# Kernel optimization log

Measured on AMD Instinct MI355X. Metric: run time of the kernel, lower is better.

The kernel has to match this reference:

```python
import jax, jax.numpy as jnp
import numpy as np

DIM = 512
DIM_HEAD = 64
HEADS = 8
SCALE = 8.0  # Attend(scale=8)
DIM_INNER = DIM_HEAD * HEADS


def setup_inputs() -> dict:
    key = jax.random.key(0)
    k1, k2, k3, k4 = jax.random.split(key, 4)
    b, n = 8, 4096
    x = jax.random.normal(k1, (b, n, DIM), dtype=jnp.float32)
    gamma = jnp.ones((DIM,), dtype=jnp.float32)
    w_qkv = jax.random.normal(k2, (DIM, 3 * DIM_INNER), dtype=jnp.float32) * (DIM ** -0.5)
    temperature = jnp.ones((HEADS, 1, 1), dtype=jnp.float32)
    w_out = jax.random.normal(k3, (DIM_INNER, DIM), dtype=jnp.float32) * (DIM_INNER ** -0.5)
    return {"x": x, "gamma": gamma, "w_qkv": w_qkv, "temperature": temperature, "w_out": w_out}


def _l2norm(t, axis=-1, eps=1e-12):
    return t / jnp.maximum(jnp.linalg.norm(t, axis=axis, keepdims=True), eps)


def reference(x, gamma, w_qkv, temperature, w_out):
    b, n, _ = x.shape
    # RMSNorm: F.normalize(x, dim=-1) * sqrt(dim) * gamma
    xn = _l2norm(x) * (DIM ** 0.5) * gamma
    qkv = xn @ w_qkv                                   # [b, n, 3*h*d]
    qkv = qkv.reshape(b, n, 3, HEADS, DIM_HEAD)
    qkv = jnp.transpose(qkv, (2, 0, 3, 4, 1))          # [3, b, h, d, n]
    q, k, v = qkv[0], qkv[1], qkv[2]
    q = _l2norm(q)                                     # l2norm over n (last dim)
    k = _l2norm(k)
    q = q * jnp.exp(temperature)                       # [h,1,1] broadcast
    sim = jnp.einsum('bhdn,bhen->bhde', q, k) * SCALE  # [b, h, d, d]
    attn = jax.nn.softmax(sim, axis=-1)
    out = jnp.einsum('bhde,bhen->bhdn', attn, v)       # [b, h, d, n]
    out = jnp.transpose(out, (0, 3, 1, 2)).reshape(b, n, DIM_INNER)
    return out @ w_out
```

## Files before the change

kernel.cpp:

```cpp
#include <hip/hip_runtime.h>
#include <stdint.h>

#define NDIM 512
#define HEADS 8
#define DHEAD 64
#define NSEQ 4096
#define BATCH 8
#define ROWS (BATCH * NSEQ)
#define QKVN (3 * NDIM)

typedef unsigned short ushort_t;
typedef __bf16 bf16x8 __attribute__((ext_vector_type(8)));
typedef float f32x4 __attribute__((ext_vector_type(4)));
typedef unsigned short u16x8 __attribute__((ext_vector_type(8)));
typedef unsigned short u16x4 __attribute__((ext_vector_type(4)));

__device__ __forceinline__ ushort_t f2bf(float f) {
  union { float f; uint32_t u; } v; v.f = f;
  uint32_t r = (v.u + 0x7FFFu + ((v.u >> 16) & 1u)) >> 16;
  return (ushort_t)r;
}
__device__ __forceinline__ float bf2f(ushort_t h) {
  union { uint32_t u; float f; } v; v.u = ((uint32_t)h) << 16;
  return v.f;
}

__device__ __forceinline__ void gload_lds16(const void* g, void* l) {
  __builtin_amdgcn_global_load_lds(
      (__attribute__((address_space(1))) void*)(g),
      (__attribute__((address_space(3))) void*)(l), 16, 0, 0);
}

__global__ __launch_bounds__(256) void prep_k(const float* __restrict__ w_qkv,
                                              const float* __restrict__ w_out,
                                              ushort_t* __restrict__ wqkvT,
                                              ushort_t* __restrict__ woutT) {
  __shared__ float tile[32][33];
  int id = blockIdx.x;
  const float* src;
  ushort_t* dst;
  int srcStride, ni, ki;
  if (id < 768) {
    ni = id % 48; ki = id / 48; src = w_qkv; dst = wqkvT; srcStride = QKVN;
  } else {
    id -= 768;
    ni = id % 16; ki = id / 16; src = w_out; dst = woutT; srcStride = NDIM;
  }
  int tr = threadIdx.x >> 3;
  int tc = (threadIdx.x & 7) * 4;
  float4 v = *(const float4*)(src + (size_t)(ki * 32 + tr) * srcStride + ni * 32 + tc);
  tile[tr][tc] = v.x; tile[tr][tc + 1] = v.y; tile[tr][tc + 2] = v.z; tile[tr][tc + 3] = v.w;
  __syncthreads();
  u16x4 o;
  o[0] = f2bf(tile[tc + 0][tr]);
  o[1] = f2bf(tile[tc + 1][tr]);
  o[2] = f2bf(tile[tc + 2][tr]);
  o[3] = f2bf(tile[tc + 3][tr]);
  *(u16x4*)(dst + (size_t)(ni * 32 + tr) * NDIM + ki * 32 + tc) = o;
}

__global__ __launch_bounds__(256) void rmsnorm_k(const float* __restrict__ x,
                                                 const float* __restrict__ gamma,
                                                 ushort_t* __restrict__ xn) {
  int wave = threadIdx.x >> 6, lane = threadIdx.x & 63;
  size_t row = (size_t)blockIdx.x * 4 + wave;
  const float4* xr = (const float4*)(x + row * NDIM);
  float4 v0 = xr[lane * 2], v1 = xr[lane * 2 + 1];
  float s = v0.x*v0.x + v0.y*v0.y + v0.z*v0.z + v0.w*v0.w
          + v1.x*v1.x + v1.y*v1.y + v1.z*v1.z + v1.w*v1.w;
#pragma unroll
  for (int off = 32; off; off >>= 1) s += __shfl_xor(s, off, 64);
  float scale = 22.627416997969522f / fmaxf(sqrtf(s), 1e-12f);
  const float4* gr = (const float4*)gamma;
  float4 g0 = gr[lane * 2], g1 = gr[lane * 2 + 1];
  u16x8 o;
  o[0] = f2bf(v0.x * scale * g0.x);
  o[1] = f2bf(v0.y * scale * g0.y);
  o[2] = f2bf(v0.z * scale * g0.z);
  o[3] = f2bf(v0.w * scale * g0.w);
  o[4] = f2bf(v1.x * scale * g1.x);
  o[5] = f2bf(v1.y * scale * g1.y);
  o[6] = f2bf(v1.z * scale * g1.z);
  o[7] = f2bf(v1.w * scale * g1.w);
  *(u16x8*)(xn + row * NDIM + lane * 8) = o;
}

template <bool OUT_BF16>
__device__ __forceinline__ void gemm256x128_core(
    const ushort_t* __restrict__ A, size_t strideA, size_t m0,
    const ushort_t* __restrict__ B,
    void* __restrict__ C, size_t strideC, size_t n0,
    ushort_t* sm) {
  const int tid  = threadIdx.x;
  const int lane = tid & 63;
  const int wave = tid >> 6;
  const int srow = lane >> 3;
  const int scol = ((lane & 7) ^ srow) * 16;
  const int r = lane & 15, q = lane >> 4;
  const int wm = (wave >> 1) * 64;
  const int wn = (wave & 1) * 64;

  ushort_t* As = sm;
  ushort_t* Bs = sm + 49152;

  auto stageA = [&](int t2, int g) {
    gload_lds16((const char*)(A + (m0 + (size_t)(g * 8 + srow)) * strideA + t2 * 64) + scol,
                (char*)(As + (t2 % 3) * 16384 + g * 512));
  };
  auto stageB = [&](int t2, int g) {
    gload_lds16((const char*)(B + (size_t)(g * 8 + srow) * NDIM + t2 * 64) + scol,
                (char*)(Bs + (t2 % 3) * 8192 + g * 512));
  };

#pragma unroll
  for (int t2 = 0; t2 < 2; ++t2) {
#pragma unroll
    for (int a = 0; a < 4; ++a) stageA(t2, wave * 4 + a);
#pragma unroll
    for (int bb = 0; bb < 2; ++bb) stageB(t2, wave * 2 + bb);
  }
  asm volatile("s_waitcnt vmcnt(6)" ::: "memory");
  __builtin_amdgcn_s_barrier();

  f32x4 acc[4][4] = {};

#pragma unroll
  for (int t = 0; t < 8; ++t) {
    const ushort_t* Ab = As + (t % 3) * 16384;
    const ushort_t* Bb = Bs + (t % 3) * 8192;
#pragma unroll
    for (int ph = 0; ph < 2; ++ph) {
      const int kb = ph * 4 + q;
      bf16x8 af[4], bfr[4];
#pragma unroll
      for (int i = 0; i < 4; ++i) {
        int row = wm + i * 16 + r;
        af[i] = *(const bf16x8*)(const void*)(Ab + row * 64 + ((kb ^ (row & 7)) << 3));
      }
#pragma unroll
      for (int j = 0; j < 4; ++j) {
        int row = wn + j * 16 + r;
        bfr[j] = *(const bf16x8*)(const void*)(Bb + row * 64 + ((kb ^ (row & 7)) << 3));
      }
      if (t < 6) {
        int t2 = t + 2;
        if (ph == 0) { stageA(t2, wave * 4 + 0); stageA(t2, wave * 4 + 1); stageB(t2, wave * 2 + 0); }
        else         { stageA(t2, wave * 4 + 2); stageA(t2, wave * 4 + 3); stageB(t2, wave * 2 + 1); }
      }
      __builtin_amdgcn_s_barrier();
      asm volatile("s_waitcnt lgkmcnt(0)" ::: "memory");
      __builtin_amdgcn_s_setprio(1);
#pragma unroll
      for (int i = 0; i < 4; ++i)
#pragma unroll
        for (int j = 0; j < 4; ++j)
          acc[i][j] = __builtin_amdgcn_mfma_f32_16x16x32_bf16(af[i], bfr[j], acc[i][j], 0, 0, 0);
      __builtin_amdgcn_s_setprio(0);
      if (ph == 1) {
        if (t < 6)       { asm volatile("s_waitcnt vmcnt(6)" ::: "memory"); }
        else if (t == 6) { asm volatile("s_waitcnt vmcnt(0)" ::: "memory"); }
      }
      __builtin_amdgcn_s_barrier();
    }
  }

  __syncthreads();
  if constexpr (OUT_BF16) {
    ushort_t* Cb = sm;
    ushort_t* Cc = (ushort_t*)C;
#pragma unroll
    for (int i = 0; i < 4; ++i)
#pragma unroll
      for (int j = 0; j < 4; ++j)
#pragma unroll
        for (int v = 0; v < 4; ++v)
          Cb[(wm + i * 16 + q * 4 + v) * 136 + wn + j * 16 + r] = f2bf(acc[i][j][v]);
    __syncthreads();
#pragma unroll
    for (int it = 0; it < 8; ++it) {
      int row = (tid >> 4) + it * 32;
      int col = (tid & 15) * 8;
      u16x8 val = *(const u16x8*)(Cb + row * 136 + col);
      *(u16x8*)(Cc + (m0 + row) * strideC + n0 + col) = val;
    }
  } else {
    float* Cf = (float*)sm;
    float* Co = (float*)C;
#pragma unroll
    for (int p = 0; p < 2; ++p) {
      __syncthreads();
      if (((wave >> 2) & 1) == p) {
#pragma unroll
        for (int i = 0; i < 4; ++i)
#pragma unroll
          for (int j = 0; j < 4; ++j)
#pragma unroll
            for (int v = 0; v < 4; ++v)
              Cf[((wm & 127) + i * 16 + q * 4 + v) * 132 + wn + j * 16 + r] = acc[i][j][v];
      }
      __syncthreads();
      int row = tid >> 2;
      int c0 = (tid & 3) * 4;
#pragma unroll
      for (int it = 0; it < 8; ++it) {
        int col = c0 + it * 16;
        f32x4 val = *(const f32x4*)(Cf + row * 132 + col);
        *(f32x4*)(Co + (m0 + p * 128 + row) * strideC + n0 + col) = val;
      }
    }
  }
}

__global__ __launch_bounds__(512, 2) void gemm_qkv(const ushort_t* __restrict__ A,
                                                   const ushort_t* __restrict__ BT,
                                                   ushort_t* __restrict__ C) {
  __shared__ __align__(16) ushort_t sm[73728];
  const int flat = blockIdx.x;
  const int xcd = flat & 7;
  const int idx = flat >> 3;
  const int local_m = idx / 12;
  const int n_t = idx - local_m * 12;
  const size_t m0 = (size_t)(xcd * 16 + local_m) * 256;
  const size_t n0 = (size_t)n_t * 128;
  gemm256x128_core<true>(A, NDIM, m0, BT + n0 * NDIM, C, QKVN, n0, sm);
}

__global__ __launch_bounds__(256) void gram_k(const ushort_t* __restrict__ qkv,
                                              float* __restrict__ pG,
                                              float* __restrict__ pSq) {
  int chunk = blockIdx.x;
  int bh = blockIdx.y;
  int b = bh >> 3, h = bh & 7;
  __shared__ ushort_t Qt[64 * 72];
  __shared__ ushort_t Kt[64 * 72];
  __shared__ float sq[128];
  int tid = threadIdx.x, lane = tid & 63, wave = tid >> 6;
  int nl = tid >> 2;
  int dp = (tid & 3) * 16;
  int r = lane & 15, q = lane >> 4;
  float aq[16] = {}, ak[16] = {};
  f32x4 acc[4] = {};
  size_t base_row = ((size_t)b * NSEQ + (size_t)chunk * 512) * QKVN + (size_t)h * DHEAD;
  int swz_n = ((nl >> 3) & 7);
  int c_lo = (nl & 7) | (((swz_n ^ (dp >> 3)) & 7) << 3);
  int c_hi = (nl & 7) | (((swz_n ^ ((dp >> 3) + 1)) & 7) << 3);
  ushort_t* qlo = Qt + dp * 72 + c_lo;
  ushort_t* qhi = Qt + (dp + 8) * 72 + c_hi;
  ushort_t* klo = Kt + dp * 72 + c_lo;
  ushort_t* khi = Kt + (dp + 8) * 72 + c_hi;

  for (int sc = 0; sc < 8; ++sc) {
    __syncthreads();
    size_t g = base_row + (size_t)(sc * 64 + nl) * QKVN;
    u16x8 qv0 = *(const u16x8*)(qkv + g + dp);
    u16x8 qv1 = *(const u16x8*)(qkv + g + dp + 8);
    u16x8 kv0 = *(const u16x8*)(qkv + g + NDIM + dp);
    u16x8 kv1 = *(const u16x8*)(qkv + g + NDIM + dp + 8);
#pragma unroll
    for (int i = 0; i < 8; ++i) {
      float fq = bf2f(qv0[i]); aq[i] += fq * fq;       qlo[i * 72] = qv0[i];
      float fq2 = bf2f(qv1[i]); aq[8 + i] += fq2 * fq2; qhi[i * 72] = qv1[i];
      float fk = bf2f(kv0[i]); ak[i] += fk * fk;       klo[i * 72] = kv0[i];
      float fk2 = bf2f(kv1[i]); ak[8 + i] += fk2 * fk2; khi[i * 72] = kv1[i];
    }
    __syncthreads();
#pragma unroll
    for (int ks = 0; ks < 64; ks += 32) {
      int kb = (ks >> 3) + q;
      int m = wave * 16 + r;
      bf16x8 a = *(const bf16x8*)(const void*)(Qt + m * 72 + (((kb ^ (m >> 3)) & 7) << 3));
#pragma unroll
      for (int j = 0; j < 4; ++j) {
        int e = j * 16 + r;
        bf16x8 bb = *(const bf16x8*)(const void*)(Kt + e * 72 + (((kb ^ (e >> 3)) & 7) << 3));
        acc[j] = __builtin_amdgcn_mfma_f32_16x16x32_bf16(a, bb, acc[j], 0, 0, 0);
      }
    }
  }
  size_t gbase = ((size_t)bh * 8 + chunk) * 4096;
#pragma unroll
  for (int j = 0; j < 4; ++j)
#pragma unroll
    for (int v = 0; v < 4; ++v)
      pG[gbase + (size_t)(wave * 16 + q * 4 + v) * 64 + j * 16 + r] = acc[j][v];
  if (tid < 128) sq[tid] = 0.f;
  __syncthreads();
#pragma unroll
  for (int i = 0; i < 16; ++i) {
    atomicAdd(&sq[dp + i], aq[i]);
    atomicAdd(&sq[64 + dp + i], ak[i]);
  }
  __syncthreads();
  if (tid < 128) pSq[((size_t)bh * 8 + chunk) * 128 + tid] = sq[tid];
}

__global__ __launch_bounds__(256) void softmax_k(const float* __restrict__ pG,
                                                 const float* __restrict__ pSq,
                                                 const float* __restrict__ temp,
                                                 ushort_t* __restrict__ attnT) {
  int bh = blockIdx.x;
  int h = bh & 7;
  int t = threadIdx.x;
  int d = t >> 2;
  int eg = (t & 3) * 16;
  __shared__ float kn[64];
  if (t < 64) {
    float sk = 0.f;
    for (int c = 0; c < 8; ++c) sk += pSq[((size_t)bh * 8 + c) * 128 + 64 + t];
    kn[t] = fmaxf(sqrtf(sk), 1e-12f);
  }
  float sq = 0.f;
  for (int c = 0; c < 8; ++c) sq += pSq[((size_t)bh * 8 + c) * 128 + d];
  float qn = fmaxf(sqrtf(sq), 1e-12f);
  __syncthreads();
  float scale = 8.0f * expf(temp[h]) / qn;
  float row[16];
#pragma unroll
  for (int k = 0; k < 16; ++k) row[k] = 0.f;
  for (int c = 0; c < 8; ++c) {
    const float4* src = (const float4*)(pG + ((size_t)bh * 8 + c) * 4096 + d * 64 + eg);
#pragma unroll
    for (int k4 = 0; k4 < 4; ++k4) {
      float4 v = src[k4];
      row[k4 * 4 + 0] += v.x; row[k4 * 4 + 1] += v.y;
      row[k4 * 4 + 2] += v.z; row[k4 * 4 + 3] += v.w;
    }
  }
#pragma unroll
  for (int k = 0; k < 16; ++k) row[k] = row[k] * scale / kn[eg + k];
  float mx = -1e30f;
#pragma unroll
  for (int k = 0; k < 16; ++k) mx = fmaxf(mx, row[k]);
  mx = fmaxf(mx, __shfl_xor(mx, 1, 64));
  mx = fmaxf(mx, __shfl_xor(mx, 2, 64));
  float s = 0.f;
#pragma unroll
  for (int k = 0; k < 16; ++k) { row[k] = expf(row[k] - mx); s += row[k]; }
  s += __shfl_xor(s, 1, 64);
  s += __shfl_xor(s, 2, 64);
  float inv = 1.0f / s;
#pragma unroll
  for (int k = 0; k < 16; ++k)
    attnT[(size_t)bh * 4096 + (eg + k) * 64 + d] = f2bf(row[k] * inv);
}

__global__ __launch_bounds__(256) void w2t_k(const ushort_t* __restrict__ woutT,
                                             const ushort_t* __restrict__ attnT,
                                             ushort_t* __restrict__ W2T) {
  int mq = blockIdx.x;
  int bh = blockIdx.y;
  int b = bh >> 3, h = bh & 7;
  int tid = threadIdx.x, lane = tid & 63, wave = tid >> 6;
  int r = lane & 15, q = lane >> 4;
  int mbase = mq * 128 + wave * 32;
  const ushort_t* At = attnT + (size_t)bh * 4096;
  f32x4 acc[2][4] = {};
#pragma unroll
  for (int kk = 0; kk < 64; kk += 32) {
    bf16x8 a[2], bb[4];
#pragma unroll
    for (int mf = 0; mf < 2; ++mf)
      a[mf] = *(const bf16x8*)(woutT + (size_t)(mbase + mf * 16 + r) * NDIM + h * 64 + kk + q * 8);
#pragma unroll
    for (int nf = 0; nf < 4; ++nf)
      bb[nf] = *(const bf16x8*)(At + (nf * 16 + r) * 64 + kk + q * 8);
#pragma unroll
    for (int mf = 0; mf < 2; ++mf)
#pragma unroll
      for (int nf = 0; nf < 4; ++nf)
        acc[mf][nf] = __builtin_amdgcn_mfma_f32_16x16x32_bf16(a[mf], bb[nf], acc[mf][nf], 0, 0, 0);
  }
#pragma unroll
  for (int mf = 0; mf < 2; ++mf)
#pragma unroll
    for (int nf = 0; nf < 4; ++nf)
#pragma unroll
      for (int v = 0; v < 4; ++v)
        W2T[(size_t)b * 262144 + (size_t)(mbase + mf * 16 + q * 4 + v) * NDIM +
            h * 64 + nf * 16 + r] = f2bf(acc[mf][nf][v]);
}

__global__ __launch_bounds__(512, 2) void gemm_v(const ushort_t* __restrict__ qkv,
                                                 const ushort_t* __restrict__ W2T,
                                                 float* __restrict__ out) {
  __shared__ __align__(16) ushort_t sm[73728];
  const int flat = blockIdx.x;
  const int b = flat & 7;
  const int local = flat >> 3;
  const int mt = local >> 2, nt = local & 3;
  const size_t m0 = (size_t)b * NSEQ + (size_t)mt * 256;
  const size_t n0 = (size_t)nt * 128;
  gemm256x128_core<false>(qkv + 1024, QKVN, m0,
                          W2T + (size_t)b * 262144 + n0 * NDIM,
                          out, NDIM, n0, sm);
}

extern "C" void kernel_launch(void* const* d_in, const int* in_sizes, int n_in,
                              void* d_out, int out_size, void* d_ws, size_t ws_size,
                              hipStream_t stream) {
  (void)in_sizes; (void)n_in; (void)out_size; (void)ws_size;
  const float* x     = (const float*)d_in[0];
  const float* gamma = (const float*)d_in[1];
  const float* w_qkv = (const float*)d_in[2];
  const float* temp  = (const float*)d_in[3];
  const float* w_out = (const float*)d_in[4];
  float* out = (float*)d_out;
  char* ws = (char*)d_ws;

  ushort_t* qkv   = (ushort_t*)ws;
  ushort_t* xn    = (ushort_t*)(ws + (size_t)100663296);
  float*    pG    = (float*)(ws + (size_t)100663296);
  float*    pSq   = (float*)(ws + (size_t)100663296 + 8388608);
  ushort_t* W2T   = (ushort_t*)(ws + (size_t)100663296 + 12582912);
  ushort_t* wqkvT = (ushort_t*)(ws + (size_t)134217728);
  ushort_t* woutT = (ushort_t*)(ws + (size_t)134217728 + 1572864);
  ushort_t* attnT = (ushort_t*)(ws + (size_t)134217728 + 2097152);

  prep_k<<<1024, 256, 0, stream>>>(w_qkv, w_out, wqkvT, woutT);
  rmsnorm_k<<<ROWS / 4, 256, 0, stream>>>(x, gamma, xn);
  gemm_qkv<<<(QKVN / 128) * (ROWS / 256), 512, 0, stream>>>(xn, wqkvT, qkv);
  gram_k<<<dim3(8, 64), 256, 0, stream>>>(qkv, pG, pSq);
  softmax_k<<<64, 256, 0, stream>>>(pG, pSq, temp, attnT);
  w2t_k<<<dim3(4, 64), 256, 0, stream>>>(woutT, attnT, W2T);
  gemm_v<<<(NDIM / 128) * (ROWS / 256), 512, 0, stream>>>(qkv, W2T, out);
}
```

Before: 260.2 us.

## Reassociate attention via per-batch Gram matrix of normalized input, skipping QKV projection

Instead of materializing the full QKV projection (32K x 1536), the pipeline computes the per-batch covariance S = xn^T xn with a split-K atomic GEMM. It then derives the q/k Gram and the norms from Wq^T S Wk and the diagonal terms, and folds attention, Wv and Wout into one 512x512 matrix per batch. The output becomes a single GEMM of xn against that fused matrix. This removes the large QKV GEMM and the associated memory traffic, at the cost of an extra transpose of xn, fp32 atomics, and bf16 rounding of S, which changes numerical accuracy.

```diff
diff --git a/kernel.cpp b/kernel.cpp
--- a/kernel.cpp
+++ b/kernel.cpp
@@ -31,65 +31,103 @@
       (__attribute__((address_space(3))) void*)(l), 16, 0, 0);
 }
 
-__global__ __launch_bounds__(256) void prep_k(const float* __restrict__ w_qkv,
-                                              const float* __restrict__ w_out,
-                                              ushort_t* __restrict__ wqkvT,
-                                              ushort_t* __restrict__ woutT) {
+__global__ __launch_bounds__(256) void prep_rms_k(const float* __restrict__ x,
+                                                  const float* __restrict__ gamma,
+                                                  ushort_t* __restrict__ xn,
+                                                  const float* __restrict__ w_qkv,
+                                                  const float* __restrict__ w_out,
+                                                  ushort_t* __restrict__ wqkT,
+                                                  ushort_t* __restrict__ woutT,
+                                                  ushort_t* __restrict__ wv,
+                                                  float* __restrict__ S) {
   __shared__ float tile[32][33];
-  int id = blockIdx.x;
-  const float* src;
-  ushort_t* dst;
-  int srcStride, ni, ki;
-  if (id < 768) {
-    ni = id % 48; ki = id / 48; src = w_qkv; dst = wqkvT; srcStride = QKVN;
+  int bid = blockIdx.x;
+  int t = threadIdx.x;
+  if (bid < 8192) {
+    int wave = t >> 6, lane = t & 63;
+    size_t row = (size_t)bid * 4 + wave;
+    const float4* xr = (const float4*)(x + row * NDIM);
+    float4 v0 = xr[lane * 2], v1 = xr[lane * 2 + 1];
+    float s = v0.x*v0.x + v0.y*v0.y + v0.z*v0.z + v0.w*v0.w
+            + v1.x*v1.x + v1.y*v1.y + v1.z*v1.z + v1.w*v1.w;
+#pragma unroll
+    for (int off = 32; off; off >>= 1) s += __shfl_xor(s, off, 64);
+    float scale = 22.627416997969522f / fmaxf(sqrtf(s), 1e-12f);
+    const float4* gr = (const float4*)gamma;
+    float4 g0 = gr[lane * 2], g1 = gr[lane * 2 + 1];
+    u16x8 o;
+    o[0] = f2bf(v0.x * scale * g0.x);
+    o[1] = f2bf(v0.y * scale * g0.y);
+    o[2] = f2bf(v0.z * scale * g0.z);
+    o[3] = f2bf(v0.w * scale * g0.w);
+    o[4] = f2bf(v1.x * scale * g1.x);
+    o[5] = f2bf(v1.y * scale * g1.y);
+    o[6] = f2bf(v1.z * scale * g1.z);
+    o[7] = f2bf(v1.w * scale * g1.w);
+    *(u16x8*)(xn + row * NDIM + lane * 8) = o;
+  } else if (bid < 8960) {
+    int id = bid - 8192;
+    const float* src;
+    ushort_t* dst;
+    int srcStride, ni, ki;
+    if (id < 512) { ni = id & 31; ki = id >> 5; src = w_qkv; dst = wqkT; srcStride = QKVN; }
+    else { id -= 512; ni = id & 15; ki = id >> 4; src = w_out; dst = woutT; srcStride = NDIM; }
+    int tr = t >> 3;
+    int tc = (t & 7) * 4;
+    float4 v = *(const float4*)(src + (size_t)(ki * 32 + tr) * srcStride + ni * 32 + tc);
+    tile[tr][tc] = v.x; tile[tr][tc + 1] = v.y; tile[tr][tc + 2] = v.z; tile[tr][tc + 3] = v.w;
+    __syncthreads();
+    u16x4 o;
+    o[0] = f2bf(tile[tc + 0][tr]);
+    o[1] = f2bf(tile[tc + 1][tr]);
+    o[2] = f2bf(tile[tc + 2][tr]);
+    o[3] = f2bf(tile[tc + 3][tr]);
+    *(u16x4*)(dst + (size_t)(ni * 32 + tr) * NDIM + ki * 32 + tc) = o;
+  } else if (bid < 9088) {
+    int id = bid - 8960;
+    int f = id * 2048 + t * 8;
+    int c = f >> 9, j = f & 511;
+    float4 u0 = *(const float4*)(w_qkv + (size_t)c * QKVN + 1024 + j);
+    float4 u1 = *(const float4*)(w_qkv + (size_t)c * QKVN + 1024 + j + 4);
+    u16x8 o;
+    o[0] = f2bf(u0.x); o[1] = f2bf(u0.y); o[2] = f2bf(u0.z); o[3] = f2bf(u0.w);
+    o[4] = f2bf(u1.x); o[5] = f2bf(u1.y); o[6] = f2bf(u1.z); o[7] = f2bf(u1.w);
+    *(u16x8*)(wv + (size_t)c * 512 + j) = o;
   } else {
-    id -= 768;
-    ni = id % 16; ki = id / 16; src = w_out; dst = woutT; srcStride = NDIM;
-  }
-  int tr = threadIdx.x >> 3;
-  int tc = (threadIdx.x & 7) * 4;
-  float4 v = *(const float4*)(src + (size_t)(ki * 32 + tr) * srcStride + ni * 32 + tc);
-  tile[tr][tc] = v.x; tile[tr][tc + 1] = v.y; tile[tr][tc + 2] = v.z; tile[tr][tc + 3] = v.w;
+    int id = bid - 9088;
+    f32x4 z = {};
+#pragma unroll
+    for (int i = 0; i < 4; ++i)
+      *(f32x4*)(S + (size_t)id * 4096 + i * 1024 + t * 4) = z;
+  }
+}
+
+__global__ __launch_bounds__(256) void xnt_k(const ushort_t* __restrict__ xn,
+                                             ushort_t* __restrict__ xnT) {
+  __shared__ ushort_t tile[64 * 72];
+  int nt = blockIdx.x & 511, ct = blockIdx.x >> 9;
+  int n0 = nt * 64, c0 = ct * 64;
+  int t = threadIdx.x;
+  int row = t >> 2, cc = (t & 3) * 16;
+  *(u16x8*)(tile + row * 72 + cc)     = *(const u16x8*)(xn + (size_t)(n0 + row) * NDIM + c0 + cc);
+  *(u16x8*)(tile + row * 72 + cc + 8) = *(const u16x8*)(xn + (size_t)(n0 + row) * NDIM + c0 + cc + 8);
   __syncthreads();
-  u16x4 o;
-  o[0] = f2bf(tile[tc + 0][tr]);
-  o[1] = f2bf(tile[tc + 1][tr]);
-  o[2] = f2bf(tile[tc + 2][tr]);
-  o[3] = f2bf(tile[tc + 3][tr]);
-  *(u16x4*)(dst + (size_t)(ni * 32 + tr) * NDIM + ki * 32 + tc) = o;
-}
-
-__global__ __launch_bounds__(256) void rmsnorm_k(const float* __restrict__ x,
-                                                 const float* __restrict__ gamma,
-                                                 ushort_t* __restrict__ xn) {
-  int wave = threadIdx.x >> 6, lane = threadIdx.x & 63;
-  size_t row = (size_t)blockIdx.x * 4 + wave;
-  const float4* xr = (const float4*)(x + row * NDIM);
-  float4 v0 = xr[lane * 2], v1 = xr[lane * 2 + 1];
-  float s = v0.x*v0.x + v0.y*v0.y + v0.z*v0.z + v0.w*v0.w
-          + v1.x*v1.x + v1.y*v1.y + v1.z*v1.z + v1.w*v1.w;
-#pragma unroll
-  for (int off = 32; off; off >>= 1) s += __shfl_xor(s, off, 64);
-  float scale = 22.627416997969522f / fmaxf(sqrtf(s), 1e-12f);
-  const float4* gr = (const float4*)gamma;
-  float4 g0 = gr[lane * 2], g1 = gr[lane * 2 + 1];
-  u16x8 o;
-  o[0] = f2bf(v0.x * scale * g0.x);
-  o[1] = f2bf(v0.y * scale * g0.y);
-  o[2] = f2bf(v0.z * scale * g0.z);
-  o[3] = f2bf(v0.w * scale * g0.w);
-  o[4] = f2bf(v1.x * scale * g1.x);
-  o[5] = f2bf(v1.y * scale * g1.y);
-  o[6] = f2bf(v1.z * scale * g1.z);
-  o[7] = f2bf(v1.w * scale * g1.w);
-  *(u16x8*)(xn + row * NDIM + lane * 8) = o;
-}
-
-template <bool OUT_BF16>
-__device__ __forceinline__ void gemm256x128_core(
+  int oc = t >> 2, on = (t & 3) * 16;
+  u16x8 a, b;
+#pragma unroll
+  for (int i = 0; i < 8; ++i) {
+    a[i] = tile[(on + i) * 72 + oc];
+    b[i] = tile[(on + 8 + i) * 72 + oc];
+  }
+  *(u16x8*)(xnT + (size_t)(c0 + oc) * ROWS + n0 + on)     = a;
+  *(u16x8*)(xnT + (size_t)(c0 + oc) * ROWS + n0 + on + 8) = b;
+}
+
+template <int NT, int OMODE>
+__device__ __forceinline__ void ring_core(
     const ushort_t* __restrict__ A, size_t strideA, size_t m0,
-    const ushort_t* __restrict__ B,
-    void* __restrict__ C, size_t strideC, size_t n0,
+    const ushort_t* __restrict__ B, size_t strideB,
+    float* __restrict__ C, size_t strideC, size_t crow0, size_t n0,
     ushort_t* sm) {
   const int tid  = threadIdx.x;
   const int lane = tid & 63;
@@ -108,7 +146,7 @@
                 (char*)(As + (t2 % 3) * 16384 + g * 512));
   };
   auto stageB = [&](int t2, int g) {
-    gload_lds16((const char*)(B + (size_t)(g * 8 + srow) * NDIM + t2 * 64) + scol,
+    gload_lds16((const char*)(B + (size_t)(g * 8 + srow) * strideB + t2 * 64) + scol,
                 (char*)(Bs + (t2 % 3) * 8192 + g * 512));
   };
 
@@ -125,7 +163,7 @@
   f32x4 acc[4][4] = {};
 
 #pragma unroll
-  for (int t = 0; t < 8; ++t) {
+  for (int t = 0; t < NT; ++t) {
     const ushort_t* Ab = As + (t % 3) * 16384;
     const ushort_t* Bb = Bs + (t % 3) * 8192;
 #pragma unroll
@@ -142,7 +180,7 @@
         int row = wn + j * 16 + r;
         bfr[j] = *(const bf16x8*)(const void*)(Bb + row * 64 + ((kb ^ (row & 7)) << 3));
       }
-      if (t < 6) {
+      if (t < NT - 2) {
         int t2 = t + 2;
         if (ph == 0) { stageA(t2, wave * 4 + 0); stageA(t2, wave * 4 + 1); stageB(t2, wave * 2 + 0); }
         else         { stageA(t2, wave * 4 + 2); stageA(t2, wave * 4 + 3); stageB(t2, wave * 2 + 1); }
@@ -157,35 +195,24 @@
           acc[i][j] = __builtin_amdgcn_mfma_f32_16x16x32_bf16(af[i], bfr[j], acc[i][j], 0, 0, 0);
       __builtin_amdgcn_s_setprio(0);
       if (ph == 1) {
-        if (t < 6)       { asm volatile("s_waitcnt vmcnt(6)" ::: "memory"); }
-        else if (t == 6) { asm volatile("s_waitcnt vmcnt(0)" ::: "memory"); }
+        if (t < NT - 2)       { asm volatile("s_waitcnt vmcnt(6)" ::: "memory"); }
+        else if (t == NT - 2) { asm volatile("s_waitcnt vmcnt(0)" ::: "memory"); }
       }
       __builtin_amdgcn_s_barrier();
     }
   }
 
-  __syncthreads();
-  if constexpr (OUT_BF16) {
-    ushort_t* Cb = sm;
-    ushort_t* Cc = (ushort_t*)C;
+  if constexpr (OMODE == 2) {
 #pragma unroll
     for (int i = 0; i < 4; ++i)
 #pragma unroll
       for (int j = 0; j < 4; ++j)
 #pragma unroll
         for (int v = 0; v < 4; ++v)
-          Cb[(wm + i * 16 + q * 4 + v) * 136 + wn + j * 16 + r] = f2bf(acc[i][j][v]);
-    __syncthreads();
-#pragma unroll
-    for (int it = 0; it < 8; ++it) {
-      int row = (tid >> 4) + it * 32;
-      int col = (tid & 15) * 8;
-      u16x8 val = *(const u16x8*)(Cb + row * 136 + col);
-      *(u16x8*)(Cc + (m0 + row) * strideC + n0 + col) = val;
-    }
+          atomicAdd(&C[(crow0 + wm + i * 16 + q * 4 + v) * strideC + n0 + wn + j * 16 + r],
+                    acc[i][j][v]);
   } else {
     float* Cf = (float*)sm;
-    float* Co = (float*)C;
 #pragma unroll
     for (int p = 0; p < 2; ++p) {
       __syncthreads();
@@ -205,129 +232,154 @@
       for (int it = 0; it < 8; ++it) {
         int col = c0 + it * 16;
         f32x4 val = *(const f32x4*)(Cf + row * 132 + col);
-        *(f32x4*)(Co + (m0 + p * 128 + row) * strideC + n0 + col) = val;
-      }
-    }
-  }
-}
-
-__global__ __launch_bounds__(512, 2) void gemm_qkv(const ushort_t* __restrict__ A,
-                                                   const ushort_t* __restrict__ BT,
-                                                   ushort_t* __restrict__ C) {
+        *(f32x4*)(C + (crow0 + p * 128 + row) * strideC + n0 + col) = val;
+      }
+    }
+  }
+}
+
+__global__ __launch_bounds__(512, 2) void syrk_k(const ushort_t* __restrict__ xnT,
+                                                 float* __restrict__ S) {
   __shared__ __align__(16) ushort_t sm[73728];
   const int flat = blockIdx.x;
-  const int xcd = flat & 7;
-  const int idx = flat >> 3;
-  const int local_m = idx / 12;
-  const int n_t = idx - local_m * 12;
-  const size_t m0 = (size_t)(xcd * 16 + local_m) * 256;
-  const size_t n0 = (size_t)n_t * 128;
-  gemm256x128_core<true>(A, NDIM, m0, BT + n0 * NDIM, C, QKVN, n0, sm);
-}
-
-__global__ __launch_bounds__(256) void gram_k(const ushort_t* __restrict__ qkv,
-                                              float* __restrict__ pG,
-                                              float* __restrict__ pSq) {
-  int chunk = blockIdx.x;
-  int bh = blockIdx.y;
+  const int b = flat & 7;
+  const int local = flat >> 3;
+  const int ks = local & 3;
+  const int tl = local >> 2;
+  const int mt = tl >> 2, nt = tl & 3;
+  const size_t m0 = (size_t)mt * 256;
+  const size_t n0 = (size_t)nt * 128;
+  const ushort_t* Abase = xnT + (size_t)b * NSEQ + (size_t)ks * 1024;
+  ring_core<16, 2>(Abase, ROWS, m0,
+                   Abase + n0 * ROWS, ROWS,
+                   S + (size_t)b * 262144, 512, m0, n0, sm);
+}
+
+__global__ __launch_bounds__(256) void pt_k(const ushort_t* __restrict__ wqkT,
+                                            const float* __restrict__ S,
+                                            ushort_t* __restrict__ PT) {
+  __shared__ __align__(16) ushort_t As[8192];
+  __shared__ __align__(16) ushort_t Bs[8192];
+  const int flat = blockIdx.x;
+  const int b = flat & 7;
+  const int local = flat >> 3;
+  const int mt = local >> 2, nt = local & 3;
+  const int m0 = mt * 128, n0 = nt * 128;
+  const int tid = threadIdx.x;
+  const int lane = tid & 63, wave = tid >> 6;
+  const int srow = lane >> 3;
+  const int scol = ((lane & 7) ^ srow) * 16;
+  const int r = lane & 15, q = lane >> 4;
+  const int wm = (wave >> 1) * 64, wn = (wave & 1) * 64;
+  const float* Sb = S + (size_t)b * 262144;
+  const int brow = tid >> 1, bhalf = tid & 1;
+
+  f32x4 acc[4][4] = {};
+  for (int k0 = 0; k0 < 512; k0 += 64) {
+    __syncthreads();
+#pragma unroll
+    for (int c = 0; c < 4; ++c) {
+      int g = wave * 4 + c;
+      gload_lds16((const char*)(wqkT + (size_t)(m0 + g * 8 + srow) * 512 + k0) + scol,
+                  (char*)(As + g * 512));
+    }
+    {
+      const float* src = Sb + (size_t)(n0 + brow) * 512 + k0 + bhalf * 32;
+#pragma unroll
+      for (int u = 0; u < 4; ++u) {
+        float4 f0 = *(const float4*)(src + u * 8);
+        float4 f1 = *(const float4*)(src + u * 8 + 4);
+        u16x8 o;
+        o[0] = f2bf(f0.x); o[1] = f2bf(f0.y); o[2] = f2bf(f0.z); o[3] = f2bf(f0.w);
+        o[4] = f2bf(f1.x); o[5] = f2bf(f1.y); o[6] = f2bf(f1.z); o[7] = f2bf(f1.w);
+        int c8 = bhalf * 4 + u;
+        *(u16x8*)(Bs + brow * 64 + ((c8 ^ (brow & 7)) << 3)) = o;
+      }
+    }
+    __syncthreads();
+#pragma unroll
+    for (int ph = 0; ph < 2; ++ph) {
+      const int kb = ph * 4 + q;
+      bf16x8 af[4], bfr[4];
+#pragma unroll
+      for (int i = 0; i < 4; ++i) {
+        int row = wm + i * 16 + r;
+        af[i] = *(const bf16x8*)(const void*)(As + row * 64 + ((kb ^ (row & 7)) << 3));
+      }
+#pragma unroll
+      for (int j = 0; j < 4; ++j) {
+        int row = wn + j * 16 + r;
+        bfr[j] = *(const bf16x8*)(const void*)(Bs + row * 64 + ((kb ^ (row & 7)) << 3));
+      }
+#pragma unroll
+      for (int i = 0; i < 4; ++i)
+#pragma unroll
+        for (int j = 0; j < 4; ++j)
+          acc[i][j] = __builtin_amdgcn_mfma_f32_16x16x32_bf16(af[i], bfr[j], acc[i][j], 0, 0, 0);
+    }
+  }
+  ushort_t* dst = PT + (size_t)b * 524288;
+#pragma unroll
+  for (int i = 0; i < 4; ++i)
+#pragma unroll
+    for (int j = 0; j < 4; ++j)
+#pragma unroll
+      for (int v = 0; v < 4; ++v)
+        dst[(size_t)(m0 + wm + i * 16 + q * 4 + v) * 512 + n0 + wn + j * 16 + r] =
+            f2bf(acc[i][j][v]);
+}
+
+__global__ __launch_bounds__(256) void gsm_k(const ushort_t* __restrict__ wqkT,
+                                             const ushort_t* __restrict__ PT,
+                                             const float* __restrict__ temp,
+                                             ushort_t* __restrict__ attnT) {
+  int bh = blockIdx.x;
   int b = bh >> 3, h = bh & 7;
-  __shared__ ushort_t Qt[64 * 72];
-  __shared__ ushort_t Kt[64 * 72];
-  __shared__ float sq[128];
-  int tid = threadIdx.x, lane = tid & 63, wave = tid >> 6;
-  int nl = tid >> 2;
-  int dp = (tid & 3) * 16;
+  int hb = h * 64;
+  __shared__ float Gf[64][68];
+  __shared__ float kq[128];
+  int t = threadIdx.x, lane = t & 63, wave = t >> 6;
   int r = lane & 15, q = lane >> 4;
-  float aq[16] = {}, ak[16] = {};
+  const ushort_t* ptb = PT + (size_t)b * 524288;
+
   f32x4 acc[4] = {};
-  size_t base_row = ((size_t)b * NSEQ + (size_t)chunk * 512) * QKVN + (size_t)h * DHEAD;
-  int swz_n = ((nl >> 3) & 7);
-  int c_lo = (nl & 7) | (((swz_n ^ (dp >> 3)) & 7) << 3);
-  int c_hi = (nl & 7) | (((swz_n ^ ((dp >> 3) + 1)) & 7) << 3);
-  ushort_t* qlo = Qt + dp * 72 + c_lo;
-  ushort_t* qhi = Qt + (dp + 8) * 72 + c_hi;
-  ushort_t* klo = Kt + dp * 72 + c_lo;
-  ushort_t* khi = Kt + (dp + 8) * 72 + c_hi;
-
-  for (int sc = 0; sc < 8; ++sc) {
-    __syncthreads();
-    size_t g = base_row + (size_t)(sc * 64 + nl) * QKVN;
-    u16x8 qv0 = *(const u16x8*)(qkv + g + dp);
-    u16x8 qv1 = *(const u16x8*)(qkv + g + dp + 8);
-    u16x8 kv0 = *(const u16x8*)(qkv + g + NDIM + dp);
-    u16x8 kv1 = *(const u16x8*)(qkv + g + NDIM + dp + 8);
-#pragma unroll
-    for (int i = 0; i < 8; ++i) {
-      float fq = bf2f(qv0[i]); aq[i] += fq * fq;       qlo[i * 72] = qv0[i];
-      float fq2 = bf2f(qv1[i]); aq[8 + i] += fq2 * fq2; qhi[i * 72] = qv1[i];
-      float fk = bf2f(kv0[i]); ak[i] += fk * fk;       klo[i * 72] = kv0[i];
-      float fk2 = bf2f(kv1[i]); ak[8 + i] += fk2 * fk2; khi[i * 72] = kv1[i];
-    }
-    __syncthreads();
-#pragma unroll
-    for (int ks = 0; ks < 64; ks += 32) {
-      int kb = (ks >> 3) + q;
-      int m = wave * 16 + r;
-      bf16x8 a = *(const bf16x8*)(const void*)(Qt + m * 72 + (((kb ^ (m >> 3)) & 7) << 3));
-#pragma unroll
-      for (int j = 0; j < 4; ++j) {
-        int e = j * 16 + r;
-        bf16x8 bb = *(const bf16x8*)(const void*)(Kt + e * 72 + (((kb ^ (e >> 3)) & 7) << 3));
-        acc[j] = __builtin_amdgcn_mfma_f32_16x16x32_bf16(a, bb, acc[j], 0, 0, 0);
-      }
-    }
-  }
-  size_t gbase = ((size_t)bh * 8 + chunk) * 4096;
+  const ushort_t* arow = wqkT + (size_t)(hb + wave * 16 + r) * 512;
+#pragma unroll
+  for (int kk = 0; kk < 512; kk += 32) {
+    bf16x8 a = *(const bf16x8*)(arow + kk + q * 8);
+#pragma unroll
+    for (int j = 0; j < 4; ++j) {
+      bf16x8 bb = *(const bf16x8*)(ptb + (size_t)(512 + hb + j * 16 + r) * 512 + kk + q * 8);
+      acc[j] = __builtin_amdgcn_mfma_f32_16x16x32_bf16(a, bb, acc[j], 0, 0, 0);
+    }
+  }
 #pragma unroll
   for (int j = 0; j < 4; ++j)
 #pragma unroll
     for (int v = 0; v < 4; ++v)
-      pG[gbase + (size_t)(wave * 16 + q * 4 + v) * 64 + j * 16 + r] = acc[j][v];
-  if (tid < 128) sq[tid] = 0.f;
+      Gf[wave * 16 + q * 4 + v][j * 16 + r] = acc[j][v];
+  if (t < 128) {
+    int row = (t < 64) ? (hb + t) : (512 + hb + (t - 64));
+    const ushort_t* wr = wqkT + (size_t)row * 512;
+    const ushort_t* pr = ptb + (size_t)row * 512;
+    float s = 0.f;
+    for (int i = 0; i < 512; i += 8) {
+      u16x8 wa = *(const u16x8*)(wr + i);
+      u16x8 pa = *(const u16x8*)(pr + i);
+#pragma unroll
+      for (int e2 = 0; e2 < 8; ++e2) s += bf2f(wa[e2]) * bf2f(pa[e2]);
+    }
+    kq[t] = s;
+  }
   __syncthreads();
-#pragma unroll
-  for (int i = 0; i < 16; ++i) {
-    atomicAdd(&sq[dp + i], aq[i]);
-    atomicAdd(&sq[64 + dp + i], ak[i]);
-  }
-  __syncthreads();
-  if (tid < 128) pSq[((size_t)bh * 8 + chunk) * 128 + tid] = sq[tid];
-}
-
-__global__ __launch_bounds__(256) void softmax_k(const float* __restrict__ pG,
-                                                 const float* __restrict__ pSq,
-                                                 const float* __restrict__ temp,
-                                                 ushort_t* __restrict__ attnT) {
-  int bh = blockIdx.x;
-  int h = bh & 7;
-  int t = threadIdx.x;
-  int d = t >> 2;
-  int eg = (t & 3) * 16;
-  __shared__ float kn[64];
-  if (t < 64) {
-    float sk = 0.f;
-    for (int c = 0; c < 8; ++c) sk += pSq[((size_t)bh * 8 + c) * 128 + 64 + t];
-    kn[t] = fmaxf(sqrtf(sk), 1e-12f);
-  }
-  float sq = 0.f;
-  for (int c = 0; c < 8; ++c) sq += pSq[((size_t)bh * 8 + c) * 128 + d];
-  float qn = fmaxf(sqrtf(sq), 1e-12f);
-  __syncthreads();
+
+  int d = t >> 2, eg = (t & 3) * 16;
+  float qn = fmaxf(sqrtf(kq[d]), 1e-12f);
   float scale = 8.0f * expf(temp[h]) / qn;
   float row[16];
 #pragma unroll
-  for (int k = 0; k < 16; ++k) row[k] = 0.f;
-  for (int c = 0; c < 8; ++c) {
-    const float4* src = (const float4*)(pG + ((size_t)bh * 8 + c) * 4096 + d * 64 + eg);
-#pragma unroll
-    for (int k4 = 0; k4 < 4; ++k4) {
-      float4 v = src[k4];
-      row[k4 * 4 + 0] += v.x; row[k4 * 4 + 1] += v.y;
-      row[k4 * 4 + 2] += v.z; row[k4 * 4 + 3] += v.w;
-    }
-  }
-#pragma unroll
-  for (int k = 0; k < 16; ++k) row[k] = row[k] * scale / kn[eg + k];
+  for (int k = 0; k < 16; ++k)
+    row[k] = Gf[d][eg + k] * scale / fmaxf(sqrtf(kq[64 + eg + k]), 1e-12f);
   float mx = -1e30f;
 #pragma unroll
   for (int k = 0; k < 16; ++k) mx = fmaxf(mx, row[k]);
@@ -344,45 +396,76 @@
     attnT[(size_t)bh * 4096 + (eg + k) * 64 + d] = f2bf(row[k] * inv);
 }
 
-__global__ __launch_bounds__(256) void w2t_k(const ushort_t* __restrict__ woutT,
-                                             const ushort_t* __restrict__ attnT,
-                                             ushort_t* __restrict__ W2T) {
-  int mq = blockIdx.x;
-  int bh = blockIdx.y;
-  int b = bh >> 3, h = bh & 7;
-  int tid = threadIdx.x, lane = tid & 63, wave = tid >> 6;
+__global__ __launch_bounds__(256) void atmt_k(const ushort_t* __restrict__ woutT,
+                                              const ushort_t* __restrict__ attnT,
+                                              const ushort_t* __restrict__ wv,
+                                              ushort_t* __restrict__ MT) {
+  __shared__ ushort_t at[128 * 72];
+  const int flat = blockIdx.x;
+  const int b = flat & 7;
+  const int local = flat >> 3;
+  const int mq = local >> 2, nq = local & 3;
+  int t = threadIdx.x, lane = t & 63, w = t >> 6;
   int r = lane & 15, q = lane >> 4;
-  int mbase = mq * 128 + wave * 32;
-  const ushort_t* At = attnT + (size_t)bh * 4096;
-  f32x4 acc[2][4] = {};
-#pragma unroll
-  for (int kk = 0; kk < 64; kk += 32) {
-    bf16x8 a[2], bb[4];
-#pragma unroll
-    for (int mf = 0; mf < 2; ++mf)
-      a[mf] = *(const bf16x8*)(woutT + (size_t)(mbase + mf * 16 + r) * NDIM + h * 64 + kk + q * 8);
-#pragma unroll
-    for (int nf = 0; nf < 4; ++nf)
-      bb[nf] = *(const bf16x8*)(At + (nf * 16 + r) * 64 + kk + q * 8);
-#pragma unroll
-    for (int mf = 0; mf < 2; ++mf)
-#pragma unroll
-      for (int nf = 0; nf < 4; ++nf)
-        acc[mf][nf] = __builtin_amdgcn_mfma_f32_16x16x32_bf16(a[mf], bb[nf], acc[mf][nf], 0, 0, 0);
-  }
-#pragma unroll
-  for (int mf = 0; mf < 2; ++mf)
-#pragma unroll
-    for (int nf = 0; nf < 4; ++nf)
+  int wm2 = (w >> 1) * 64, wn2 = (w & 1) * 64;
+  f32x4 acc2[4][4] = {};
+  for (int h = 0; h < 8; ++h) {
+    int hb = h * 64;
+    const ushort_t* atn = attnT + (size_t)(b * 8 + h) * 4096;
+    f32x4 acc1[2][4] = {};
+#pragma unroll
+    for (int kk = 0; kk < 64; kk += 32) {
+      bf16x8 a[2], bb[4];
+#pragma unroll
+      for (int i = 0; i < 2; ++i)
+        a[i] = *(const bf16x8*)(woutT + (size_t)(mq * 128 + w * 32 + i * 16 + r) * 512 + hb + kk + q * 8);
+#pragma unroll
+      for (int j = 0; j < 4; ++j)
+        bb[j] = *(const bf16x8*)(atn + (j * 16 + r) * 64 + kk + q * 8);
+#pragma unroll
+      for (int i = 0; i < 2; ++i)
+#pragma unroll
+        for (int j = 0; j < 4; ++j)
+          acc1[i][j] = __builtin_amdgcn_mfma_f32_16x16x32_bf16(a[i], bb[j], acc1[i][j], 0, 0, 0);
+    }
+    __syncthreads();
+#pragma unroll
+    for (int i = 0; i < 2; ++i)
+#pragma unroll
+      for (int j = 0; j < 4; ++j)
+#pragma unroll
+        for (int v = 0; v < 4; ++v)
+          at[(w * 32 + i * 16 + q * 4 + v) * 72 + j * 16 + r] = f2bf(acc1[i][j][v]);
+    __syncthreads();
+#pragma unroll
+    for (int kk = 0; kk < 64; kk += 32) {
+      bf16x8 a2[4], b2[4];
+#pragma unroll
+      for (int i = 0; i < 4; ++i)
+        a2[i] = *(const bf16x8*)(const void*)(at + (wm2 + i * 16 + r) * 72 + kk + q * 8);
+#pragma unroll
+      for (int j = 0; j < 4; ++j)
+        b2[j] = *(const bf16x8*)(wv + (size_t)(nq * 128 + wn2 + j * 16 + r) * 512 + hb + kk + q * 8);
+#pragma unroll
+      for (int i = 0; i < 4; ++i)
+#pragma unroll
+        for (int j = 0; j < 4; ++j)
+          acc2[i][j] = __builtin_amdgcn_mfma_f32_16x16x32_bf16(a2[i], b2[j], acc2[i][j], 0, 0, 0);
+    }
+  }
+#pragma unroll
+  for (int i = 0; i < 4; ++i)
+#pragma unroll
+    for (int j = 0; j < 4; ++j)
 #pragma unroll
       for (int v = 0; v < 4; ++v)
-        W2T[(size_t)b * 262144 + (size_t)(mbase + mf * 16 + q * 4 + v) * NDIM +
-            h * 64 + nf * 16 + r] = f2bf(acc[mf][nf][v]);
-}
-
-__global__ __launch_bounds__(512, 2) void gemm_v(const ushort_t* __restrict__ qkv,
-                                                 const ushort_t* __restrict__ W2T,
-                                                 float* __restrict__ out) {
+        MT[(size_t)b * 262144 + (size_t)(mq * 128 + wm2 + i * 16 + q * 4 + v) * 512 +
+           nq * 128 + wn2 + j * 16 + r] = f2bf(acc2[i][j][v]);
+}
+
+__global__ __launch_bounds__(512, 2) void final_k(const ushort_t* __restrict__ xn,
+                                                  const ushort_t* __restrict__ MT,
+                                                  float* __restrict__ out) {
   __shared__ __align__(16) ushort_t sm[73728];
   const int flat = blockIdx.x;
   const int b = flat & 7;
@@ -390,9 +473,9 @@
   const int mt = local >> 2, nt = local & 3;
   const size_t m0 = (size_t)b * NSEQ + (size_t)mt * 256;
   const size_t n0 = (size_t)nt * 128;
-  gemm256x128_core<false>(qkv + 1024, QKVN, m0,
-                          W2T + (size_t)b * 262144 + n0 * NDIM,
-                          out, NDIM, n0, sm);
+  ring_core<8, 1>(xn, NDIM, m0,
+                  MT + (size_t)b * 262144 + n0 * 512, 512,
+                  out, NDIM, m0, n0, sm);
 }
 
 extern "C" void kernel_launch(void* const* d_in, const int* in_sizes, int n_in,
@@ -407,20 +490,21 @@
   float* out = (float*)d_out;
   char* ws = (char*)d_ws;
 
-  ushort_t* qkv   = (ushort_t*)ws;
-  ushort_t* xn    = (ushort_t*)(ws + (size_t)100663296);
-  float*    pG    = (float*)(ws + (size_t)100663296);
-  float*    pSq   = (float*)(ws + (size_t)100663296 + 8388608);
-  ushort_t* W2T   = (ushort_t*)(ws + (size_t)100663296 + 12582912);
-  ushort_t* wqkvT = (ushort_t*)(ws + (size_t)134217728);
-  ushort_t* woutT = (ushort_t*)(ws + (size_t)134217728 + 1572864);
-  ushort_t* attnT = (ushort_t*)(ws + (size_t)134217728 + 2097152);
-
-  prep_k<<<1024, 256, 0, stream>>>(w_qkv, w_out, wqkvT, woutT);
-  rmsnorm_k<<<ROWS / 4, 256, 0, stream>>>(x, gamma, xn);
-  gemm_qkv<<<(QKVN / 128) * (ROWS / 256), 512, 0, stream>>>(xn, wqkvT, qkv);
-  gram_k<<<dim3(8, 64), 256, 0, stream>>>(qkv, pG, pSq);
-  softmax_k<<<64, 256, 0, stream>>>(pG, pSq, temp, attnT);
-  w2t_k<<<dim3(4, 64), 256, 0, stream>>>(woutT, attnT, W2T);
-  gemm_v<<<(NDIM / 128) * (ROWS / 256), 512, 0, stream>>>(qkv, W2T, out);
-}
+  ushort_t* xn    = (ushort_t*)ws;
+  ushort_t* xnT   = (ushort_t*)(ws + (size_t)33554432);
+  float*    S     = (float*)   (ws + (size_t)67108864);
+  ushort_t* PT    = (ushort_t*)(ws + (size_t)75497472);
+  ushort_t* MT    = (ushort_t*)(ws + (size_t)83886080);
+  ushort_t* attnT = (ushort_t*)(ws + (size_t)88080384);
+  ushort_t* wqkT  = (ushort_t*)(ws + (size_t)88604672);
+  ushort_t* woutT = (ushort_t*)(ws + (size_t)89653248);
+  ushort_t* wv    = (ushort_t*)(ws + (size_t)90177536);
+
+  prep_rms_k<<<9600, 256, 0, stream>>>(x, gamma, xn, w_qkv, w_out, wqkT, woutT, wv, S);
+  xnt_k<<<4096, 256, 0, stream>>>(xn, xnT);
+  syrk_k<<<256, 512, 0, stream>>>(xnT, S);
+  pt_k<<<256, 256, 0, stream>>>(wqkT, S, PT);
+  gsm_k<<<64, 256, 0, stream>>>(wqkT, PT, temp, attnT);
+  atmt_k<<<128, 256, 0, stream>>>(woutT, attnT, wv, MT);
+  final_k<<<512, 512, 0, stream>>>(xn, MT, out);
+}
```

Measured after the change: 271.5 us. 4.3% more time.
